# Optimization experiments

Hardware: AMD Instinct MI355X
Metric: run time of the kernel (lower is better)

## Reference

```python
import jax, jax.numpy as jnp
import numpy as np

N_NODES = 100000
N_EDGES = 1600000
IN_C, HID_C, OUT_C = 64, 128, 64


def _sage_conv(x, src, dst, Wl, bl, Wr, n_nodes):
    # PyG SAGEConv (mean aggr): out = lin_l(mean_{j in N(i)} x_j) + lin_r(x_i)
    msg = x[src]  # [E, C] gather
    agg = jax.ops.segment_sum(msg, dst, num_segments=n_nodes)
    deg = jax.ops.segment_sum(jnp.ones((src.shape[0],), x.dtype), dst, num_segments=n_nodes)
    agg = agg / jnp.maximum(deg, 1.0)[:, None]
    return agg @ Wl + bl + x @ Wr


def setup_inputs() -> dict:
    key = jax.random.key(0)
    ks = jax.random.split(key, 16)
    x = jax.random.normal(ks[0], (N_NODES, IN_C), dtype=jnp.float32)
    edge_index = jax.random.randint(ks[1], (2, N_EDGES), 0, N_NODES, dtype=jnp.int64)
    s = 0.05
    return {
        "x": x,
        "edge_index": edge_index,
        # conv1: SAGEConv(IN_C, HID_C)
        "Wl1": jax.random.normal(ks[2], (IN_C, HID_C), jnp.float32) * s,
        "bl1": jnp.zeros((HID_C,), jnp.float32),
        "Wr1": jax.random.normal(ks[3], (IN_C, HID_C), jnp.float32) * s,
        # conv2: SAGEConv(HID_C, OUT_C)
        "Wl2": jax.random.normal(ks[4], (HID_C, OUT_C), jnp.float32) * s,
        "bl2": jnp.zeros((OUT_C,), jnp.float32),
        "Wr2": jax.random.normal(ks[5], (HID_C, OUT_C), jnp.float32) * s,
        # classifier MLP: OUT_C -> HID_C -> HID_C//2 -> 1
        "Wc1": jax.random.normal(ks[6], (OUT_C, HID_C), jnp.float32) * s,
        "bc1": jnp.zeros((HID_C,), jnp.float32),
        "Wc2": jax.random.normal(ks[7], (HID_C, HID_C // 2), jnp.float32) * s,
        "bc2": jnp.zeros((HID_C // 2,), jnp.float32),
        "Wc3": jax.random.normal(ks[8], (HID_C // 2, 1), jnp.float32) * s,
        "bc3": jnp.zeros((1,), jnp.float32),
    }


def reference(x, edge_index, Wl1, bl1, Wr1, Wl2, bl2, Wr2, Wc1, bc1, Wc2, bc2, Wc3, bc3):
    src, dst = edge_index[0], edge_index[1]
    n = x.shape[0]
    h = _sage_conv(x, src, dst, Wl1, bl1, Wr1, n)
    h = jax.nn.relu(h)  # dropout is identity in eval mode
    embeddings = _sage_conv(h, src, dst, Wl2, bl2, Wr2, n)
    # classifier head
    c = jax.nn.relu(embeddings @ Wc1 + bc1)
    c = jax.nn.relu(c @ Wc2 + bc2)
    fraud_probs = jax.nn.sigmoid(c @ Wc3 + bc3)
    return embeddings, fraud_probs
```

## Files before the change

kernel.cpp:

```cpp
#include <hip/hip_runtime.h>
#include <math.h>

#define N_NODES 100000
#define ZERO_NODE 100000
#define N_EDGES 1600000
#define NBKT    391
#define BCAP    5120
#define EPB     4096
#define NBLKA   391
#define PADBKT  768
#define BUCKET_CAP (N_EDGES + NBKT * PADBKT + BCAP)

using short8  = __attribute__((ext_vector_type(8))) short;
using float4v = __attribute__((ext_vector_type(4))) float;

__device__ inline unsigned short f2bf(float f) {
    unsigned int u = __float_as_uint(f);
    u += 0x7fffu + ((u >> 16) & 1u);
    return (unsigned short)(u >> 16);
}
__device__ inline float bflo(unsigned int v) { return __uint_as_float(v << 16); }
__device__ inline float bfhi(unsigned int v) { return __uint_as_float(v & 0xffff0000u); }

__global__ void prep_all(const float* __restrict__ x, unsigned short* __restrict__ xb,
                         const float* __restrict__ Wl1, const float* __restrict__ Wr1,
                         const float* __restrict__ Wl2, const float* __restrict__ Wr2,
                         const float* __restrict__ Wc1, const float* __restrict__ Wc2,
                         unsigned short* __restrict__ w1, unsigned short* __restrict__ w2,
                         unsigned short* __restrict__ wcls1, unsigned short* __restrict__ wcls2,
                         unsigned short* __restrict__ t2b) {
    int bid = blockIdx.x;
    int t = threadIdx.x;
    if (bid < 6250) {
        int i = bid * 256 + t;
        float4 v = *(const float4*)(x + (long)i * 4);
        uint2 o;
        o.x = (unsigned)f2bf(v.x) | ((unsigned)f2bf(v.y) << 16);
        o.y = (unsigned)f2bf(v.z) | ((unsigned)f2bf(v.w) << 16);
        *(uint2*)(xb + (long)i * 4) = o;
    } else if (bid < 6442) {
        int i = (bid - 6250) * 256 + t;
        if (i < 16384) {
            int n = i >> 7, k = i & 127;
            float v = (k < 64) ? Wl1[k * 128 + n] : Wr1[(k - 64) * 128 + n];
            w1[i] = f2bf(v);
        } else if (i < 32768) {
            int j = i - 16384; int n = j >> 7, k = j & 127;
            float v = (n < 64) ? Wl2[k * 64 + n] : Wr2[k * 64 + (n - 64)];
            w2[j] = f2bf(v);
        } else if (i < 40960) {
            int j = i - 32768; int n = j >> 6, k = j & 63;
            wcls1[j] = f2bf(Wc1[k * 128 + n]);
        } else {
            int j = i - 40960; int n = j >> 7, k = j & 127;
            wcls2[j] = f2bf(Wc2[k * 64 + n]);
        }
    } else {
        if (t < 32)       ((unsigned*)(xb  + (long)ZERO_NODE * 64))[t]      = 0u;
        else if (t < 64)  ((unsigned*)(t2b + (long)ZERO_NODE * 64))[t - 32] = 0u;
    }
}

__global__ __launch_bounds__(256) void binA(const int* __restrict__ esrc,
                                            const int* __restrict__ edst,
                                            int* __restrict__ bcnt,
                                            unsigned* __restrict__ stage) {
    __shared__ int hist[NBKT];
    __shared__ int rbase[NBKT];
    int t = threadIdx.x;
    for (int i = t; i < NBKT; i += 256) hist[i] = 0;
    __syncthreads();
    int e0 = blockIdx.x * EPB;
    int e1 = e0 + EPB; if (e1 > N_EDGES) e1 = N_EDGES;
    unsigned pk[16];
    int bn[16];
#pragma unroll
    for (int j = 0; j < 16; j++) {
        int e = e0 + j * 256 + t;
        bn[j] = -1;
        if (e < N_EDGES && e < e1) {
            int d = edst[e];
            int s = esrc[e];
            int b = d >> 8;
            pk[j] = (unsigned)s | ((unsigned)(d & 255) << 24);
            bn[j] = b;
            atomicAdd(&hist[b], 1);
        }
    }
    __syncthreads();
    for (int i = t; i < NBKT; i += 256) {
        int c = hist[i];
        rbase[i] = c ? atomicAdd(&bcnt[i], c) : 0;
        hist[i] = 0;
    }
    __syncthreads();
#pragma unroll
    for (int j = 0; j < 16; j++) {
        if (bn[j] >= 0) {
            int b = bn[j];
            int slot = rbase[b] + atomicAdd(&hist[b], 1);
            if (slot < BCAP)
                stage[(long)b * BCAP + slot] = pk[j];
        }
    }
}

__global__ void binScan(const int* __restrict__ bcnt, int* __restrict__ pbase) {
    __shared__ int s[512];
    int t = threadIdx.x;
    int v = (t < NBKT) ? bcnt[t] : 0;
    s[t] = v;
    __syncthreads();
    for (int st = 1; st < 512; st <<= 1) {
        int a = (t >= st) ? s[t - st] : 0;
        __syncthreads();
        s[t] += a;
        __syncthreads();
    }
    if (t < NBKT) pbase[t] = (s[t] - v) + t * PADBKT;
}

__global__ __launch_bounds__(256) void binB(const int* __restrict__ bcnt,
                                            const int* __restrict__ pbase,
                                            const unsigned* __restrict__ stage,
                                            int* __restrict__ offp, int* __restrict__ deg,
                                            int* __restrict__ bucket) {
    __shared__ int hist[256];
    __shared__ int scn[256];
    __shared__ int lbase[256];
    int b = blockIdx.x, t = threadIdx.x;
    int cnt = bcnt[b];
    if (cnt > BCAP) cnt = BCAP;
    int base = pbase[b];
    hist[t] = 0;
    __syncthreads();
    const unsigned* sp = stage + (long)b * BCAP;
    unsigned pk[20];
    int nv = 0;
#pragma unroll
    for (int j = 0; j < 20; j++) {
        int i = j * 256 + t;
        if (i < cnt) {
            pk[j] = sp[i];
            atomicAdd(&hist[pk[j] >> 24], 1);
            nv = j + 1;
        }
    }
    __syncthreads();
    int v = hist[t];
    int p4 = (v + 3) & ~3;
    scn[t] = p4;
    __syncthreads();
    for (int st = 1; st < 256; st <<= 1) {
        int a = (t >= st) ? scn[t - st] : 0;
        __syncthreads();
        scn[t] += a;
        __syncthreads();
    }
    lbase[t] = scn[t] - p4;
    int node = b * 256 + t;
    if (node < N_NODES) {
        offp[node] = base + lbase[t];
        deg[node]  = v;
    }
    hist[t] = 0;
    __syncthreads();
#pragma unroll
    for (int j = 0; j < 20; j++) {
        if (j < nv) {
            unsigned p = pk[j];
            int ln = p >> 24;
            int slot = atomicAdd(&hist[ln], 1);
            bucket[base + lbase[ln] + slot] = (int)(p & 0xFFFFFFu);
        }
    }
    int ps = base + lbase[t] + v;
    int pe = base + lbase[t] + p4;
    for (int j = ps; j < pe; j++) bucket[j] = ZERO_NODE;
}

__global__ __launch_bounds__(256, 8) void gather_b(
        const unsigned short* __restrict__ y, const int* __restrict__ offp,
        const int* __restrict__ deg, const int* __restrict__ bucket,
        unsigned short* __restrict__ outb) {
    int t = threadIdx.x;
    int wv = t >> 6, lane = t & 63;
    int nh = lane >> 5;
    int g  = (lane >> 3) & 3;
    int c8 = lane & 7;
    int node = blockIdx.x * 8 + wv * 2 + nh;
    int e0 = offp[node];
    int dg = deg[node];
    int len = (dg + 3) & ~3;
    int maxlen = max(len, __shfl_xor(len, 32));
    const char* yb = (const char*)y;
    float a[8] = {0.f, 0.f, 0.f, 0.f, 0.f, 0.f, 0.f, 0.f};
    for (int base = 0; base < maxlen; base += 16) {
        uint4 v[4];
#pragma unroll
        for (int h = 0; h < 4; h++) {
            int rel = base + h * 4 + g;
            int s = bucket[e0 + rel];
            s = (rel < len) ? s : ZERO_NODE;
            unsigned off32 = ((unsigned)s << 7) + ((unsigned)c8 << 4);
            v[h] = *(const uint4*)(yb + off32);
        }
#pragma unroll
        for (int h = 0; h < 4; h++) {
            a[0] += bflo(v[h].x); a[1] += bfhi(v[h].x);
            a[2] += bflo(v[h].y); a[3] += bfhi(v[h].y);
            a[4] += bflo(v[h].z); a[5] += bfhi(v[h].z);
            a[6] += bflo(v[h].w); a[7] += bfhi(v[h].w);
        }
    }
#pragma unroll
    for (int j = 0; j < 8; j++) {
        a[j] += __shfl_xor(a[j], 8);
        a[j] += __shfl_xor(a[j], 16);
    }
    if (g == 0) {
        float sc = 1.f / fmaxf((float)dg, 1.f);
        uint4 o;
        o.x = (unsigned)f2bf(a[0]*sc) | ((unsigned)f2bf(a[1]*sc) << 16);
        o.y = (unsigned)f2bf(a[2]*sc) | ((unsigned)f2bf(a[3]*sc) << 16);
        o.z = (unsigned)f2bf(a[4]*sc) | ((unsigned)f2bf(a[5]*sc) << 16);
        o.w = (unsigned)f2bf(a[6]*sc) | ((unsigned)f2bf(a[7]*sc) << 16);
        *(uint4*)(outb + (long)node * 64 + c8 * 8) = o;
    }
}

__global__ __launch_bounds__(256, 8) void gather_badd(
        const unsigned short* __restrict__ y, const int* __restrict__ offp,
        const int* __restrict__ deg, const int* __restrict__ bucket,
        const unsigned short* __restrict__ ub, float* __restrict__ out) {
    int t = threadIdx.x;
    int wv = t >> 6, lane = t & 63;
    int nh = lane >> 5;
    int g  = (lane >> 3) & 3;
    int c8 = lane & 7;
    int node = blockIdx.x * 8 + wv * 2 + nh;
    int e0 = offp[node];
    int dg = deg[node];
    int len = (dg + 3) & ~3;
    int maxlen = max(len, __shfl_xor(len, 32));
    const char* yb = (const char*)y;
    float a[8] = {0.f, 0.f, 0.f, 0.f, 0.f, 0.f, 0.f, 0.f};
    for (int base = 0; base < maxlen; base += 16) {
        uint4 v[4];
#pragma unroll
        for (int h = 0; h < 4; h++) {
            int rel = base + h * 4 + g;
            int s = bucket[e0 + rel];
            s = (rel < len) ? s : ZERO_NODE;
            unsigned off32 = ((unsigned)s << 7) + ((unsigned)c8 << 4);
            v[h] = *(const uint4*)(yb + off32);
        }
#pragma unroll
        for (int h = 0; h < 4; h++) {
            a[0] += bflo(v[h].x); a[1] += bfhi(v[h].x);
            a[2] += bflo(v[h].y); a[3] += bfhi(v[h].y);
            a[4] += bflo(v[h].z); a[5] += bfhi(v[h].z);
            a[6] += bflo(v[h].w); a[7] += bfhi(v[h].w);
        }
    }
#pragma unroll
    for (int j = 0; j < 8; j++) {
        a[j] += __shfl_xor(a[j], 8);
        a[j] += __shfl_xor(a[j], 16);
    }
    if (g == 0) {
        float sc = 1.f / fmaxf((float)dg, 1.f);
        uint2 uv = *(const uint2*)(ub + (long)node * 64 + c8 * 8);
        float4 r0 = { a[0]*sc + bflo(uv.x), a[1]*sc + bfhi(uv.x),
                      a[2]*sc + bflo(uv.y), a[3]*sc + bfhi(uv.y) };
        uint2 uw = *(const uint2*)(ub + (long)node * 64 + c8 * 8 + 4);
        float4 r1 = { a[4]*sc + bflo(uw.x), a[5]*sc + bfhi(uw.x),
                      a[6]*sc + bflo(uw.y), a[7]*sc + bfhi(uw.y) };
        float4* op = (float4*)(out + (long)node * 64 + c8 * 8);
        op[0] = r0; op[1] = r1;
    }
}

__global__ __launch_bounds__(256, 4) void fused_conv(
        const unsigned short* __restrict__ xb, const unsigned short* __restrict__ aggb,
        const unsigned short* __restrict__ w1, const float* __restrict__ bl1,
        const unsigned short* __restrict__ w2, const float* __restrict__ bl2,
        unsigned short* __restrict__ t2b, unsigned short* __restrict__ ub) {
    __shared__ __align__(16) unsigned short smemA[64 * 136];
    __shared__ __align__(16) unsigned short smemH[64 * 136];
    unsigned short* sA = smemA;
    unsigned short* sH = smemH;
    unsigned short* stu = smemA;
    unsigned short* st2 = smemH;

    int t = threadIdx.x;
    int lane = t & 63;
    int wv = t >> 6;
    int q = lane >> 4, ln = lane & 15;

    long base = (long)blockIdx.x * 4096;
    long maxe = (long)N_NODES * 64 - 8;
#pragma unroll
    for (int it = 0; it < 2; it++) {
        int i = it * 256 + t;
        int m = i >> 3, k8 = (i & 7) * 8;
        long g = base + (long)m * 64 + k8;
        if (g > maxe) g = maxe;
        *(uint4*)(sA + m * 136 + k8)      = *(const uint4*)(aggb + g);
        *(uint4*)(sA + m * 136 + 64 + k8) = *(const uint4*)(xb + g);
    }
    __syncthreads();

    int n0 = wv * 32;
    float4v acc[2][4];
    {
        float b0 = bl1[n0 + ln], b1 = bl1[n0 + 16 + ln];
#pragma unroll
        for (int mi = 0; mi < 4; mi++) {
            acc[0][mi] = (float4v){b0, b0, b0, b0};
            acc[1][mi] = (float4v){b1, b1, b1, b1};
        }
    }
#pragma unroll
    for (int ks = 0; ks < 4; ks++) {
        int k0 = ks * 32 + q * 8;
        short8 bf0 = *(const short8*)(w1 + (long)(n0 + ln) * 128 + k0);
        short8 bf1 = *(const short8*)(w1 + (long)(n0 + 16 + ln) * 128 + k0);
#pragma unroll
        for (int mi = 0; mi < 4; mi++) {
            short8 af = *(const short8*)(sA + (mi * 16 + ln) * 136 + k0);
            acc[0][mi] = __builtin_amdgcn_mfma_f32_16x16x32_bf16(af, bf0, acc[0][mi], 0, 0, 0);
            acc[1][mi] = __builtin_amdgcn_mfma_f32_16x16x32_bf16(af, bf1, acc[1][mi], 0, 0, 0);
        }
    }
#pragma unroll
    for (int j = 0; j < 2; j++)
#pragma unroll
        for (int mi = 0; mi < 4; mi++) {
            int n = n0 + j * 16 + ln;
#pragma unroll
            for (int r = 0; r < 4; r++) {
                int m = mi * 16 + q * 4 + r;
                sH[m * 136 + n] = f2bf(fmaxf(acc[j][mi][r], 0.f));
            }
        }
    __syncthreads();

    float4v acc2[2][4];
    {
        float c0 = (n0 >= 64) ? bl2[n0 - 64 + ln] : 0.f;
        float c1 = (n0 >= 64) ? bl2[n0 - 48 + ln] : 0.f;
#pragma unroll
        for (int mi = 0; mi < 4; mi++) {
            acc2[0][mi] = (float4v){c0, c0, c0, c0};
            acc2[1][mi] = (float4v){c1, c1, c1, c1};
        }
    }
#pragma unroll
    for (int ks = 0; ks < 4; ks++) {
        int k0 = ks * 32 + q * 8;
        short8 bf0 = *(const short8*)(w2 + (long)(n0 + ln) * 128 + k0);
        short8 bf1 = *(const short8*)(w2 + (long)(n0 + 16 + ln) * 128 + k0);
#pragma unroll
        for (int mi = 0; mi < 4; mi++) {
            short8 af = *(const short8*)(sH + (mi * 16 + ln) * 136 + k0);
            acc2[0][mi] = __builtin_amdgcn_mfma_f32_16x16x32_bf16(af, bf0, acc2[0][mi], 0, 0, 0);
            acc2[1][mi] = __builtin_amdgcn_mfma_f32_16x16x32_bf16(af, bf1, acc2[1][mi], 0, 0, 0);
        }
    }
    __syncthreads();

#pragma unroll
    for (int j = 0; j < 2; j++)
#pragma unroll
        for (int mi = 0; mi < 4; mi++) {
            int n = n0 + j * 16 + ln;
#pragma unroll
            for (int r = 0; r < 4; r++) {
                int m = mi * 16 + q * 4 + r;
                if (wv < 2) st2[m * 72 + n] = f2bf(acc2[j][mi][r]);
                else        stu[m * 72 + (n - 64)] = f2bf(acc2[j][mi][r]);
            }
        }
    __syncthreads();

    long lim2 = (long)N_NODES * 32;
    unsigned* t2u = (unsigned*)t2b;
    unsigned* uu  = (unsigned*)ub;
    long ubase = base >> 1;
#pragma unroll
    for (int it = 0; it < 8; it++) {
        int i = it * 256 + t;
        long gq = ubase + i;
        if (gq < lim2) {
            int m = (i * 2) >> 6, n = (i * 2) & 63;
            t2u[gq] = (unsigned)st2[m * 72 + n] | ((unsigned)st2[m * 72 + n + 1] << 16);
            uu[gq]  = (unsigned)stu[m * 72 + n] | ((unsigned)stu[m * 72 + n + 1] << 16);
        }
    }
}

__global__ __launch_bounds__(256, 4) void fused_cls(
        const float* __restrict__ emb,
        const unsigned short* __restrict__ wcls1, const float* __restrict__ bc1,
        const unsigned short* __restrict__ wcls2, const float* __restrict__ bc2,
        const float* __restrict__ wc3, const float* __restrict__ bc3,
        float* __restrict__ probs) {
    __shared__ __align__(16) unsigned short smem[64 * 136];
    __shared__ float psum[4][64];
    unsigned short* sE = smem;
    unsigned short* sC = smem;

    int t = threadIdx.x;
    int wv = t >> 6;
    int lane = t & 63;
    int q = lane >> 4, ln = lane & 15;

    long base = (long)blockIdx.x * 4096;
    long maxe = (long)N_NODES * 64 - 4;
#pragma unroll
    for (int it = 0; it < 4; it++) {
        int i = it * 256 + t;
        int m = i >> 4, k4 = (i & 15) * 4;
        long g = base + (long)m * 64 + k4;
        if (g > maxe) g = maxe;
        float4 v = *(const float4*)(emb + g);
        uint2 o;
        o.x = (unsigned)f2bf(v.x) | ((unsigned)f2bf(v.y) << 16);
        o.y = (unsigned)f2bf(v.z) | ((unsigned)f2bf(v.w) << 16);
        *(uint2*)(sE + m * 72 + k4) = o;
    }
    __syncthreads();

    int n0 = wv * 32;
    float4v acc[2][4];
    {
        float b0 = bc1[n0 + ln], b1 = bc1[n0 + 16 + ln];
#pragma unroll
        for (int mi = 0; mi < 4; mi++) {
            acc[0][mi] = (float4v){b0, b0, b0, b0};
            acc[1][mi] = (float4v){b1, b1, b1, b1};
        }
    }
#pragma unroll
    for (int ks = 0; ks < 2; ks++) {
        int k0 = ks * 32 + q * 8;
        short8 bf0 = *(const short8*)(wcls1 + (long)(n0 + ln) * 64 + k0);
        short8 bf1 = *(const short8*)(wcls1 + (long)(n0 + 16 + ln) * 64 + k0);
#pragma unroll
        for (int mi = 0; mi < 4; mi++) {
            short8 af = *(const short8*)(sE + (mi * 16 + ln) * 72 + k0);
            acc[0][mi] = __builtin_amdgcn_mfma_f32_16x16x32_bf16(af, bf0, acc[0][mi], 0, 0, 0);
            acc[1][mi] = __builtin_amdgcn_mfma_f32_16x16x32_bf16(af, bf1, acc[1][mi], 0, 0, 0);
        }
    }
    __syncthreads();
#pragma unroll
    for (int j = 0; j < 2; j++)
#pragma unroll
        for (int mi = 0; mi < 4; mi++) {
            int n = n0 + j * 16 + ln;
#pragma unroll
            for (int r = 0; r < 4; r++) {
                int m = mi * 16 + q * 4 + r;
                sC[m * 136 + n] = f2bf(fmaxf(acc[j][mi][r], 0.f));
            }
        }
    __syncthreads();

    int n0c = wv * 16;
    float4v acc3[4];
    {
        float b = bc2[n0c + ln];
#pragma unroll
        for (int mi = 0; mi < 4; mi++) acc3[mi] = (float4v){b, b, b, b};
    }
#pragma unroll
    for (int ks = 0; ks < 4; ks++) {
        int k0 = ks * 32 + q * 8;
        short8 bf0 = *(const short8*)(wcls2 + (long)(n0c + ln) * 128 + k0);
#pragma unroll
        for (int mi = 0; mi < 4; mi++) {
            short8 af = *(const short8*)(sC + (mi * 16 + ln) * 136 + k0);
            acc3[mi] = __builtin_amdgcn_mfma_f32_16x16x32_bf16(af, bf0, acc3[mi], 0, 0, 0);
        }
    }
    float w3 = wc3[n0c + ln];
#pragma unroll
    for (int mi = 0; mi < 4; mi++)
#pragma unroll
        for (int r = 0; r < 4; r++) {
            float v = fmaxf(acc3[mi][r], 0.f) * w3;
            v += __shfl_xor(v, 1);
            v += __shfl_xor(v, 2);
            v += __shfl_xor(v, 4);
            v += __shfl_xor(v, 8);
            if (ln == 0) psum[wv][mi * 16 + q * 4 + r] = v;
        }
    __syncthreads();
    if (t < 64) {
        int node = blockIdx.x * 64 + t;
        if (node < N_NODES) {
            float tot = psum[0][t] + psum[1][t] + psum[2][t] + psum[3][t] + bc3[0];
            probs[node] = 1.f / (1.f + expf(-tot));
        }
    }
}

extern "C" void kernel_launch(void* const* d_in, const int* in_sizes, int n_in,
                              void* d_out, int out_size, void* d_ws, size_t ws_size,
                              hipStream_t stream) {
    const float* x   = (const float*)d_in[0];
    const int*   ei  = (const int*)d_in[1];
    const float* Wl1 = (const float*)d_in[2];
    const float* bl1 = (const float*)d_in[3];
    const float* Wr1 = (const float*)d_in[4];
    const float* Wl2 = (const float*)d_in[5];
    const float* bl2 = (const float*)d_in[6];
    const float* Wr2 = (const float*)d_in[7];
    const float* Wc1 = (const float*)d_in[8];
    const float* bc1 = (const float*)d_in[9];
    const float* Wc2 = (const float*)d_in[10];
    const float* bc2 = (const float*)d_in[11];
    const float* Wc3 = (const float*)d_in[12];
    const float* bc3 = (const float*)d_in[13];

    float* out = (float*)d_out;

    int* iw     = (int*)d_ws;
    int* bcnt   = iw;
    int* pbase  = iw + 512;
    int* offp   = iw + 1024;
    int* deg    = iw + 1024 + 100352;
    int* bucket = iw + 1024 + 2 * 100352;
    unsigned* stage = (unsigned*)(bucket + BUCKET_CAP);
    size_t ioff = ((size_t)(1024 + 2 * 100352 + BUCKET_CAP) + (size_t)NBKT * BCAP) * 4;
    ioff = (ioff + 127) & ~(size_t)127;

    char* wsb = (char*)d_ws;
    unsigned short* xb    = (unsigned short*)(wsb + ioff);
    unsigned short* agg1b = xb + 6400064L;
    unsigned short* t2b   = agg1b + 6400000L;
    unsigned short* ub    = t2b + 6400064L;
    unsigned short* w1    = ub + 6400000L;
    unsigned short* w2    = w1 + 16384;
    unsigned short* wcls1 = w2 + 16384;
    unsigned short* wcls2 = wcls1 + 8192;

    float* emb   = out;
    float* probs = out + 6400000L;

    const int* esrc = ei;
    const int* edst = ei + N_EDGES;

    hipMemsetAsync(bcnt, 0, 1024 * sizeof(int), stream);

    prep_all<<<6443, 256, 0, stream>>>(x, xb, Wl1, Wr1, Wl2, Wr2, Wc1, Wc2,
                                       w1, w2, wcls1, wcls2, t2b);

    binA<<<NBLKA, 256, 0, stream>>>(esrc, edst, bcnt, stage);
    binScan<<<1, 512, 0, stream>>>(bcnt, pbase);
    binB<<<NBKT, 256, 0, stream>>>(bcnt, pbase, stage, offp, deg, bucket);

    gather_b<<<12500, 256, 0, stream>>>(xb, offp, deg, bucket, agg1b);
    fused_conv<<<1563, 256, 0, stream>>>(xb, agg1b, w1, bl1, w2, bl2, t2b, ub);
    gather_badd<<<12500, 256, 0, stream>>>(t2b, offp, deg, bucket, ub, emb);
    fused_cls<<<1563, 256, 0, stream>>>(emb, wcls1, bc1, wcls2, bc2, Wc3, bc3, probs);
}
```

Before: 247.8 us.

## Fuse prep with binning pass and fold bucket scan into binB

Merges the conversion/weight-prep kernel with the first edge-binning pass into one launch, and removes the separate single-block scan kernel by having every binB block recompute the 391-entry prefix sum redundantly. Binning blocks now process twice as many edges each, halving the number of global atomics on bucket counts. This cuts two kernel launches and their serialization gaps, at the cost of redundant scan work per binB block and higher register use from 32-entry per-thread arrays.

```diff
diff --git a/kernel.cpp b/kernel.cpp
--- a/kernel.cpp
+++ b/kernel.cpp
@@ -6,8 +6,8 @@
 #define N_EDGES 1600000
 #define NBKT    391
 #define BCAP    5120
-#define EPB     4096
-#define NBLKA   391
+#define EPB     8192
+#define NBLKA   196
 #define PADBKT  768
 #define BUCKET_CAP (N_EDGES + NBKT * PADBKT + BCAP)
 
@@ -22,13 +22,18 @@
 __device__ inline float bflo(unsigned int v) { return __uint_as_float(v << 16); }
 __device__ inline float bfhi(unsigned int v) { return __uint_as_float(v & 0xffff0000u); }
 
-__global__ void prep_all(const float* __restrict__ x, unsigned short* __restrict__ xb,
-                         const float* __restrict__ Wl1, const float* __restrict__ Wr1,
-                         const float* __restrict__ Wl2, const float* __restrict__ Wr2,
-                         const float* __restrict__ Wc1, const float* __restrict__ Wc2,
-                         unsigned short* __restrict__ w1, unsigned short* __restrict__ w2,
-                         unsigned short* __restrict__ wcls1, unsigned short* __restrict__ wcls2,
-                         unsigned short* __restrict__ t2b) {
+__global__ __launch_bounds__(256, 4) void prep_binA(
+        const float* __restrict__ x, unsigned short* __restrict__ xb,
+        const float* __restrict__ Wl1, const float* __restrict__ Wr1,
+        const float* __restrict__ Wl2, const float* __restrict__ Wr2,
+        const float* __restrict__ Wc1, const float* __restrict__ Wc2,
+        unsigned short* __restrict__ w1, unsigned short* __restrict__ w2,
+        unsigned short* __restrict__ wcls1, unsigned short* __restrict__ wcls2,
+        unsigned short* __restrict__ t2b,
+        const int* __restrict__ esrc, const int* __restrict__ edst,
+        int* __restrict__ bcnt, unsigned* __restrict__ stage) {
+    __shared__ int hist[NBKT];
+    __shared__ int rbase[NBKT];
     int bid = blockIdx.x;
     int t = threadIdx.x;
     if (bid < 6250) {
@@ -38,7 +43,9 @@
         o.x = (unsigned)f2bf(v.x) | ((unsigned)f2bf(v.y) << 16);
         o.y = (unsigned)f2bf(v.z) | ((unsigned)f2bf(v.w) << 16);
         *(uint2*)(xb + (long)i * 4) = o;
-    } else if (bid < 6442) {
+        return;
+    }
+    if (bid < 6442) {
         int i = (bid - 6250) * 256 + t;
         if (i < 16384) {
             int n = i >> 7, k = i & 127;
@@ -55,30 +62,25 @@
             int j = i - 40960; int n = j >> 7, k = j & 127;
             wcls2[j] = f2bf(Wc2[k * 64 + n]);
         }
-    } else {
+        return;
+    }
+    if (bid == 6442) {
         if (t < 32)       ((unsigned*)(xb  + (long)ZERO_NODE * 64))[t]      = 0u;
         else if (t < 64)  ((unsigned*)(t2b + (long)ZERO_NODE * 64))[t - 32] = 0u;
-    }
-}
-
-__global__ __launch_bounds__(256) void binA(const int* __restrict__ esrc,
-                                            const int* __restrict__ edst,
-                                            int* __restrict__ bcnt,
-                                            unsigned* __restrict__ stage) {
-    __shared__ int hist[NBKT];
-    __shared__ int rbase[NBKT];
-    int t = threadIdx.x;
+        return;
+    }
+    int ab = bid - 6443;
     for (int i = t; i < NBKT; i += 256) hist[i] = 0;
     __syncthreads();
-    int e0 = blockIdx.x * EPB;
+    int e0 = ab * EPB;
     int e1 = e0 + EPB; if (e1 > N_EDGES) e1 = N_EDGES;
-    unsigned pk[16];
-    int bn[16];
-#pragma unroll
-    for (int j = 0; j < 16; j++) {
+    unsigned pk[32];
+    int bn[32];
+#pragma unroll
+    for (int j = 0; j < 32; j++) {
         int e = e0 + j * 256 + t;
         bn[j] = -1;
-        if (e < N_EDGES && e < e1) {
+        if (e < e1) {
             int d = edst[e];
             int s = esrc[e];
             int b = d >> 8;
@@ -95,7 +97,7 @@
     }
     __syncthreads();
 #pragma unroll
-    for (int j = 0; j < 16; j++) {
+    for (int j = 0; j < 32; j++) {
         if (bn[j] >= 0) {
             int b = bn[j];
             int slot = rbase[b] + atomicAdd(&hist[b], 1);
@@ -105,35 +107,29 @@
     }
 }
 
-__global__ void binScan(const int* __restrict__ bcnt, int* __restrict__ pbase) {
-    __shared__ int s[512];
-    int t = threadIdx.x;
-    int v = (t < NBKT) ? bcnt[t] : 0;
-    s[t] = v;
-    __syncthreads();
-    for (int st = 1; st < 512; st <<= 1) {
-        int a = (t >= st) ? s[t - st] : 0;
-        __syncthreads();
-        s[t] += a;
-        __syncthreads();
-    }
-    if (t < NBKT) pbase[t] = (s[t] - v) + t * PADBKT;
-}
-
 __global__ __launch_bounds__(256) void binB(const int* __restrict__ bcnt,
-                                            const int* __restrict__ pbase,
                                             const unsigned* __restrict__ stage,
                                             int* __restrict__ offp, int* __restrict__ deg,
                                             int* __restrict__ bucket) {
+    __shared__ int sg[512];
     __shared__ int hist[256];
     __shared__ int scn[256];
     __shared__ int lbase[256];
     int b = blockIdx.x, t = threadIdx.x;
-    int cnt = bcnt[b];
-    if (cnt > BCAP) cnt = BCAP;
-    int base = pbase[b];
+    sg[t]       = (t < NBKT) ? bcnt[t] : 0;
+    sg[t + 256] = (t + 256 < NBKT) ? bcnt[t + 256] : 0;
     hist[t] = 0;
     __syncthreads();
+    for (int st = 1; st < 512; st <<= 1) {
+        int a0 = (t >= st) ? sg[t - st] : 0;
+        int a1 = (t + 256 >= st) ? sg[t + 256 - st] : 0;
+        __syncthreads();
+        sg[t] += a0; sg[t + 256] += a1;
+        __syncthreads();
+    }
+    int cntraw = bcnt[b];
+    int base = (sg[b] - cntraw) + b * PADBKT;
+    int cnt = cntraw > BCAP ? BCAP : cntraw;
     const unsigned* sp = stage + (long)b * BCAP;
     unsigned pk[20];
     int nv = 0;
@@ -529,7 +525,6 @@
 
     int* iw     = (int*)d_ws;
     int* bcnt   = iw;
-    int* pbase  = iw + 512;
     int* offp   = iw + 1024;
     int* deg    = iw + 1024 + 100352;
     int* bucket = iw + 1024 + 2 * 100352;
@@ -555,12 +550,10 @@
 
     hipMemsetAsync(bcnt, 0, 1024 * sizeof(int), stream);
 
-    prep_all<<<6443, 256, 0, stream>>>(x, xb, Wl1, Wr1, Wl2, Wr2, Wc1, Wc2,
-                                       w1, w2, wcls1, wcls2, t2b);
-
-    binA<<<NBLKA, 256, 0, stream>>>(esrc, edst, bcnt, stage);
-    binScan<<<1, 512, 0, stream>>>(bcnt, pbase);
-    binB<<<NBKT, 256, 0, stream>>>(bcnt, pbase, stage, offp, deg, bucket);
+    prep_binA<<<6443 + NBLKA, 256, 0, stream>>>(x, xb, Wl1, Wr1, Wl2, Wr2, Wc1, Wc2,
+                                                w1, w2, wcls1, wcls2, t2b,
+                                                esrc, edst, bcnt, stage);
+    binB<<<NBKT, 256, 0, stream>>>(bcnt, stage, offp, deg, bucket);
 
     gather_b<<<12500, 256, 0, stream>>>(xb, offp, deg, bucket, agg1b);
     fused_conv<<<1563, 256, 0, stream>>>(xb, agg1b, w1, bl1, w2, bl2, t2b, ub);
```

Result: slower. 255.7 us (+3.2%).
